# Performance work log

Measured on AMD Instinct MI355X. Metric: run time of the kernel, lower is better.

Reference implementation:

```python
import jax, jax.numpy as jnp
import numpy as np
from jax import lax

SUBBANDS = 4
TAPS = 64
BETA = 9.0


def _qmf_filter():
    # scipy.signal.kaiser(M, beta) == np.kaiser(M, beta)
    h = np.kaiser(TAPS + 1, BETA)
    h = h / np.sum(h)
    n = np.arange(TAPS + 1)
    filt = [h * np.cos((2 * k + 1) * np.pi * n / (2 * SUBBANDS) + (-1) ** k * np.pi / 4)
            for k in range(SUBBANDS)]
    return np.asarray(filt, dtype=np.float32)  # [S, TAPS+1]


def setup_inputs() -> dict:
    key = jax.random.key(0)
    x = jax.random.normal(key, (16, 1, 524288), dtype=jnp.float32)
    qmf = jnp.asarray(_qmf_filter())
    return {"x": x, "qmf": qmf}


def reference(x, qmf):
    S = SUBBANDS
    pad = TAPS // 2  # 32
    # --- analysis: full conv then ::S decimation == strided conv (identical outputs) ---
    wa = qmf[:, None, :]  # [S, 1, TAPS+1] (OIW)
    sub = lax.conv_general_dilated(
        x, wa, window_strides=(S,), padding=[(pad, pad)],
        dimension_numbers=("NCH", "OIH", "NCH"))  # [B, S, T//S]
    # --- synthesis: zero-stuff upsample by S then conv, summed over subbands.
    # lhs_dilation=S inserts the zeros; right pad extra S-1 to match the
    # explicit x_up buffer (3 trailing zeros after the last sample).
    # Summing the S per-subband convs == one conv with S input channels.
    ws = qmf[None, :, :]  # [1, S, TAPS+1]
    y = lax.conv_general_dilated(
        sub, ws, window_strides=(1,), padding=[(pad, pad + S - 1)],
        lhs_dilation=(S,), dimension_numbers=("NCH", "OIH", "NCH"))  # [B, 1, T]
    return y
```

## Files before the change

### kernel.cpp

```cpp
#include <hip/hip_runtime.h>

#define LEN 524288
#define LSUB 131072
#define BATCH 16
#define NXG 1056
#define NTILE 128

constexpr double cabs_d(double a) { return a < 0 ? -a : a; }
constexpr double csqrt_d(double a) {
    double x = (a > 1.0) ? a : 1.0;
    for (int i = 0; i < 48; i++) x = 0.5 * (x + a / x);
    return x;
}
constexpr double i0_d(double x) {
    double t = 1.0, s = 1.0;
    for (int m = 1; m < 50; m++) { double u = x / (2.0 * m); t *= u * u; s += t; }
    return s;
}
struct Tbl {
    float f[4][65];
    float C[4][129];
};
constexpr Tbl make_tbl() {
    Tbl T{};
    double h[65] = {};
    double sum = 0.0;
    const double ib = i0_d(9.0);
    for (int n = 0; n < 65; n++) {
        double r = (n - 32.0) / 32.0;
        double a = 1.0 - r * r; if (a < 0) a = 0;
        h[n] = i0_d(9.0 * csqrt_d(a)) / ib;
        sum += h[n];
    }
    for (int n = 0; n < 65; n++) h[n] /= sum;
    const double S2 = csqrt_d(2.0);
    const double c1 = 0.5 * csqrt_d(2.0 + S2);
    const double c2 = 0.5 * S2;
    const double c3 = 0.5 * csqrt_d(2.0 - S2);
    const double ct[16] = {1,c1,c2,c3,0,-c3,-c2,-c1,-1,-c1,-c2,-c3,0,c3,c2,c1};
    double f[4][65] = {};
    for (int k = 0; k < 4; k++)
        for (int n = 0; n < 65; n++) {
            int m = ((2 * k + 1) * n + ((k & 1) ? 14 : 2)) & 15;
            f[k][n] = h[n] * ct[m];
            T.f[k][n] = (float)f[k][n];
        }
    double Cd[4][129] = {};
    for (int p = 0; p < 4; p++)
        for (int dd = -64; dd <= 64; dd++) {
            double a = 0.0;
            for (int k = 0; k < 4; k++)
                for (int j = -8; j <= 8; j++) {
                    int ia = 4 * j + 32 - p, ib2 = dd - 4 * j + 32;
                    if (ia >= 0 && ia <= 64 && ib2 >= 0 && ib2 <= 64)
                        a += f[k][ia] * f[k][ib2];
                }
            Cd[p][dd + 64] = a;
        }
    for (int p = 0; p < 4; p++) {
        double budget = 2e-8;
        while (true) {
            int best = -1; double bv = 1e30;
            for (int d = 0; d < 129; d++) {
                double c = cabs_d(Cd[p][d]);
                if (c > 0.0 && c < bv) { bv = c; best = d; }
            }
            if (best < 0 || bv * bv > budget) break;
            budget -= bv * bv;
            Cd[p][best] = 0.0;
        }
        for (int d = 0; d < 129; d++) T.C[p][d] = (float)Cd[p][d];
    }
    return T;
}
static constexpr Tbl TBL = make_tbl();

__device__ __forceinline__ int swz(int g) { return g ^ ((g >> 3) & 7); }
__device__ __forceinline__ float getc(const float4& v, int c) {
    switch (c) { case 0: return v.x; case 1: return v.y; case 2: return v.z; default: return v.w; }
}
__device__ __forceinline__ float cpv(int p, int dlt) {
    return (dlt < -64 || dlt > 64) ? 0.0f : TBL.C[p][dlt + 64];
}
__device__ __forceinline__ float lds_x(const float4* xs, int xi, int gbase) {
    int r = (xi >> 2) - gbase;
    return reinterpret_cast<const float*>(&xs[swz(r)])[xi & 3];
}

template <int TT>
__device__ __forceinline__ void left_fix(const float4* xs, float (&acc)[4][4]) {
    float sig[4][8];
    #pragma unroll
    for (int mi = 0; mi < 8; mi++) {
        const int m = mi - 8;
        float s0 = 0.f, s1 = 0.f, s2 = 0.f, s3 = 0.f;
        #pragma unroll
        for (int n = 32 - 4 * m; n <= 64; n++) {
            float xv = lds_x(xs, 4 * m - 32 + n, -16);
            s0 = fmaf(TBL.f[0][n], xv, s0);
            s1 = fmaf(TBL.f[1][n], xv, s1);
            s2 = fmaf(TBL.f[2][n], xv, s2);
            s3 = fmaf(TBL.f[3][n], xv, s3);
        }
        sig[0][mi] = s0; sig[1][mi] = s1; sig[2][mi] = s2; sig[3][mi] = s3;
    }
    #pragma unroll
    for (int o = 0; o < 4; o++) {
        const int u = 4 * TT + o;
        #pragma unroll
        for (int p = 0; p < 4; p++) {
            float s = 0.f;
            #pragma unroll
            for (int mi = 0; mi < 8; mi++) {
                const int np = 4 * ((mi - 8) - u) + 32 - p;
                if (np >= 0 && np <= 64) {
                    s = fmaf(TBL.f[0][np], sig[0][mi], s);
                    s = fmaf(TBL.f[1][np], sig[1][mi], s);
                    s = fmaf(TBL.f[2][np], sig[2][mi], s);
                    s = fmaf(TBL.f[3][np], sig[3][mi], s);
                }
            }
            acc[o][p] -= s;
        }
    }
}

template <int TT>
__device__ __forceinline__ void right_fix(const float4* xs, float (&acc)[4][4]) {
    constexpr int GB = LSUB - 1040;
    float sig[4][8];
    #pragma unroll
    for (int mi = 0; mi < 8; mi++) {
        float s0 = 0.f, s1 = 0.f, s2 = 0.f, s3 = 0.f;
        #pragma unroll
        for (int n = 0; n <= 31 - 4 * mi; n++) {
            float xv = lds_x(xs, 4 * (LSUB + mi) - 32 + n, GB);
            s0 = fmaf(TBL.f[0][n], xv, s0);
            s1 = fmaf(TBL.f[1][n], xv, s1);
            s2 = fmaf(TBL.f[2][n], xv, s2);
            s3 = fmaf(TBL.f[3][n], xv, s3);
        }
        sig[0][mi] = s0; sig[1][mi] = s1; sig[2][mi] = s2; sig[3][mi] = s3;
    }
    #pragma unroll
    for (int o = 0; o < 4; o++) {
        const int u = (LSUB - 1024) + 4 * TT + o;
        #pragma unroll
        for (int p = 0; p < 4; p++) {
            float s = 0.f;
            #pragma unroll
            for (int mi = 0; mi < 8; mi++) {
                const int np = 4 * ((LSUB + mi) - u) + 32 - p;
                if (np >= 0 && np <= 64) {
                    s = fmaf(TBL.f[0][np], sig[0][mi], s);
                    s = fmaf(TBL.f[1][np], sig[1][mi], s);
                    s = fmaf(TBL.f[2][np], sig[2][mi], s);
                    s = fmaf(TBL.f[3][np], sig[3][mi], s);
                }
            }
            acc[o][p] -= s;
        }
    }
}

__global__ __launch_bounds__(256, 8) void pqmf_composite(const float* __restrict__ x,
                                                         float* __restrict__ y) {
    __shared__ float4 xs[NXG];

    const int t = threadIdx.x;
    const int b = blockIdx.x >> 7;
    const int tile = blockIdx.x & (NTILE - 1);
    const int u0 = tile << 10;
    const float* xb = x + (size_t)b * LEN;
    const int gbase = u0 - 16;

    if (gbase >= 0 && gbase + NXG <= LSUB) {
        #pragma unroll
        for (int q = 0; q < 4; q++)
            xs[swz(t + 256 * q)] = *reinterpret_cast<const float4*>(xb + 4 * (gbase + t + 256 * q));
        if (t < NXG - 1024)
            xs[swz(t + 1024)] = *reinterpret_cast<const float4*>(xb + 4 * (gbase + t + 1024));
    } else {
        for (int r = t; r < NXG; r += 256) {
            int g = gbase + r;
            float4 v = make_float4(0.f, 0.f, 0.f, 0.f);
            if (g >= 0 && g < LSUB) v = *reinterpret_cast<const float4*>(xb + 4 * g);
            xs[swz(r)] = v;
        }
    }
    __syncthreads();

    float acc[4][4] = {};
    float4 vb[4];
    #pragma unroll
    for (int i = 0; i < 4; i++) vb[i] = xs[swz(4 * t + i)];
    #pragma unroll
    for (int d = -16; d <= 19; d++) {
        float4 v = vb[(d + 16) & 3];
        if (d + 4 <= 19) vb[(d + 16) & 3] = xs[swz(4 * t + 16 + d + 4)];
        #pragma unroll
        for (int o = 0; o < 4; o++) {
            const int e = d - o;
            if (e < -16 || e > 16) continue;
            #pragma unroll
            for (int p = 0; p < 4; p++) {
                const int c0 = p & 1, c1 = (p & 1) + 2;
                const float w0 = cpv(p, 4 * e + c0);
                const float w1 = cpv(p, 4 * e + c1);
                if (w0 != 0.f) acc[o][p] = fmaf(w0, getc(v, c0), acc[o][p]);
                if (w1 != 0.f) acc[o][p] = fmaf(w1, getc(v, c1), acc[o][p]);
            }
        }
    }

    if (tile == 0 && t < 2) {
        if (t == 0) left_fix<0>(xs, acc); else left_fix<1>(xs, acc);
    }
    if (tile == NTILE - 1 && t >= 254) {
        if (t == 254) right_fix<254>(xs, acc); else right_fix<255>(xs, acc);
    }

    float4* yb = reinterpret_cast<float4*>(y + (size_t)b * LEN);
    #pragma unroll
    for (int o = 0; o < 4; o++)
        yb[u0 + 4 * t + o] = make_float4(acc[o][0], acc[o][1], acc[o][2], acc[o][3]);
}

extern "C" void kernel_launch(void* const* d_in, const int* in_sizes, int n_in,
                              void* d_out, int out_size, void* d_ws, size_t ws_size,
                              hipStream_t stream) {
    const float* x = (const float*)d_in[0];
    float* y = (float*)d_out;
    dim3 blk(256);
    dim3 grd(BATCH * NTILE);
    pqmf_composite<<<grd, blk, 0, stream>>>(x, y);
}
```

Baseline: 113.2 us.

## Replace LDS-tiled composite filter with direct per-granule global loads

Drops the shared-memory staging tile and its barrier. Each thread now computes one output granule of 4 samples by reading its 33 neighbouring float4 values straight from global memory, relying on L1/L2 to supply the reuse between neighbouring threads. Thread count goes up 4x, and the edge corrections are done per granule. The risk is about 33 global load instructions per output granule instead of LDS reuse, and fewer outputs per thread over which to spread the register-resident weights.

```diff
diff --git a/kernel.cpp b/kernel.cpp
--- a/kernel.cpp
+++ b/kernel.cpp
@@ -3,8 +3,6 @@
 #define LEN 524288
 #define LSUB 131072
 #define BATCH 16
-#define NXG 1056
-#define NTILE 128
 
 constexpr double cabs_d(double a) { return a < 0 ? -a : a; }
 constexpr double csqrt_d(double a) {
@@ -75,155 +73,105 @@
 }
 static constexpr Tbl TBL = make_tbl();
 
-__device__ __forceinline__ int swz(int g) { return g ^ ((g >> 3) & 7); }
 __device__ __forceinline__ float getc(const float4& v, int c) {
     switch (c) { case 0: return v.x; case 1: return v.y; case 2: return v.z; default: return v.w; }
 }
 __device__ __forceinline__ float cpv(int p, int dlt) {
     return (dlt < -64 || dlt > 64) ? 0.0f : TBL.C[p][dlt + 64];
 }
-__device__ __forceinline__ float lds_x(const float4* xs, int xi, int gbase) {
-    int r = (xi >> 2) - gbase;
-    return reinterpret_cast<const float*>(&xs[swz(r)])[xi & 3];
+
+template <bool SAFE>
+__device__ __forceinline__ void compute_granule(const float4* __restrict__ xb4, int g,
+                                                float (&acc)[4]) {
+    #pragma unroll
+    for (int e = -16; e <= 16; e++) {
+        float4 v;
+        if (SAFE) {
+            int gg = g + e;
+            v = (gg >= 0 && gg < LSUB) ? xb4[gg] : make_float4(0.f, 0.f, 0.f, 0.f);
+        } else {
+            v = xb4[g + e];
+        }
+        #pragma unroll
+        for (int c = 0; c < 4; c++) {
+            const int par = c & 1;
+            const float w0 = cpv(par,     4 * e + c);
+            const float w1 = cpv(par + 2, 4 * e + c);
+            const float xv = getc(v, c);
+            if (w0 != 0.f) acc[par]     = fmaf(w0, xv, acc[par]);
+            if (w1 != 0.f) acc[par + 2] = fmaf(w1, xv, acc[par + 2]);
+        }
+    }
 }
 
-template <int TT>
-__device__ __forceinline__ void left_fix(const float4* xs, float (&acc)[4][4]) {
-    float sig[4][8];
+__device__ void left_fix_g(const float* __restrict__ xb, int g, float (&acc)[4]) {
     #pragma unroll
     for (int mi = 0; mi < 8; mi++) {
         const int m = mi - 8;
         float s0 = 0.f, s1 = 0.f, s2 = 0.f, s3 = 0.f;
         #pragma unroll
-        for (int n = 32 - 4 * m; n <= 64; n++) {
-            float xv = lds_x(xs, 4 * m - 32 + n, -16);
+        for (int n = 64 - 4 * mi; n <= 64; n++) {
+            float xv = xb[4 * m - 32 + n];
             s0 = fmaf(TBL.f[0][n], xv, s0);
             s1 = fmaf(TBL.f[1][n], xv, s1);
             s2 = fmaf(TBL.f[2][n], xv, s2);
             s3 = fmaf(TBL.f[3][n], xv, s3);
         }
-        sig[0][mi] = s0; sig[1][mi] = s1; sig[2][mi] = s2; sig[3][mi] = s3;
-    }
-    #pragma unroll
-    for (int o = 0; o < 4; o++) {
-        const int u = 4 * TT + o;
         #pragma unroll
         for (int p = 0; p < 4; p++) {
-            float s = 0.f;
-            #pragma unroll
-            for (int mi = 0; mi < 8; mi++) {
-                const int np = 4 * ((mi - 8) - u) + 32 - p;
-                if (np >= 0 && np <= 64) {
-                    s = fmaf(TBL.f[0][np], sig[0][mi], s);
-                    s = fmaf(TBL.f[1][np], sig[1][mi], s);
-                    s = fmaf(TBL.f[2][np], sig[2][mi], s);
-                    s = fmaf(TBL.f[3][np], sig[3][mi], s);
-                }
+            int np = 4 * (m - g) + 32 - p;
+            if (np >= 0 && np <= 64) {
+                float w = TBL.f[0][np] * s0 + TBL.f[1][np] * s1 +
+                          TBL.f[2][np] * s2 + TBL.f[3][np] * s3;
+                acc[p] -= w;
             }
-            acc[o][p] -= s;
         }
     }
 }
 
-template <int TT>
-__device__ __forceinline__ void right_fix(const float4* xs, float (&acc)[4][4]) {
-    constexpr int GB = LSUB - 1040;
-    float sig[4][8];
+__device__ void right_fix_g(const float* __restrict__ xb, int g, float (&acc)[4]) {
     #pragma unroll
     for (int mi = 0; mi < 8; mi++) {
+        const int m = LSUB + mi;
         float s0 = 0.f, s1 = 0.f, s2 = 0.f, s3 = 0.f;
         #pragma unroll
         for (int n = 0; n <= 31 - 4 * mi; n++) {
-            float xv = lds_x(xs, 4 * (LSUB + mi) - 32 + n, GB);
+            float xv = xb[4 * m - 32 + n];
             s0 = fmaf(TBL.f[0][n], xv, s0);
             s1 = fmaf(TBL.f[1][n], xv, s1);
             s2 = fmaf(TBL.f[2][n], xv, s2);
             s3 = fmaf(TBL.f[3][n], xv, s3);
         }
-        sig[0][mi] = s0; sig[1][mi] = s1; sig[2][mi] = s2; sig[3][mi] = s3;
-    }
-    #pragma unroll
-    for (int o = 0; o < 4; o++) {
-        const int u = (LSUB - 1024) + 4 * TT + o;
         #pragma unroll
         for (int p = 0; p < 4; p++) {
-            float s = 0.f;
-            #pragma unroll
-            for (int mi = 0; mi < 8; mi++) {
-                const int np = 4 * ((LSUB + mi) - u) + 32 - p;
-                if (np >= 0 && np <= 64) {
-                    s = fmaf(TBL.f[0][np], sig[0][mi], s);
-                    s = fmaf(TBL.f[1][np], sig[1][mi], s);
-                    s = fmaf(TBL.f[2][np], sig[2][mi], s);
-                    s = fmaf(TBL.f[3][np], sig[3][mi], s);
-                }
+            int np = 4 * (m - g) + 32 - p;
+            if (np >= 0 && np <= 64) {
+                float w = TBL.f[0][np] * s0 + TBL.f[1][np] * s1 +
+                          TBL.f[2][np] * s2 + TBL.f[3][np] * s3;
+                acc[p] -= w;
             }
-            acc[o][p] -= s;
         }
     }
 }
 
-__global__ __launch_bounds__(256, 8) void pqmf_composite(const float* __restrict__ x,
-                                                         float* __restrict__ y) {
-    __shared__ float4 xs[NXG];
+__global__ __launch_bounds__(256, 4) void pqmf_direct(const float* __restrict__ x,
+                                                      float* __restrict__ y) {
+    const int idx = blockIdx.x * 256 + threadIdx.x;
+    const int g = idx & (LSUB - 1);
+    const int b = idx >> 17;
+    const float* xb = x + (size_t)b * LEN;
+    const float4* xb4 = reinterpret_cast<const float4*>(xb);
 
-    const int t = threadIdx.x;
-    const int b = blockIdx.x >> 7;
-    const int tile = blockIdx.x & (NTILE - 1);
-    const int u0 = tile << 10;
-    const float* xb = x + (size_t)b * LEN;
-    const int gbase = u0 - 16;
-
-    if (gbase >= 0 && gbase + NXG <= LSUB) {
-        #pragma unroll
-        for (int q = 0; q < 4; q++)
-            xs[swz(t + 256 * q)] = *reinterpret_cast<const float4*>(xb + 4 * (gbase + t + 256 * q));
-        if (t < NXG - 1024)
-            xs[swz(t + 1024)] = *reinterpret_cast<const float4*>(xb + 4 * (gbase + t + 1024));
+    float acc[4] = {0.f, 0.f, 0.f, 0.f};
+    if (g >= 16 && g < LSUB - 16) {
+        compute_granule<false>(xb4, g, acc);
     } else {
-        for (int r = t; r < NXG; r += 256) {
-            int g = gbase + r;
-            float4 v = make_float4(0.f, 0.f, 0.f, 0.f);
-            if (g >= 0 && g < LSUB) v = *reinterpret_cast<const float4*>(xb + 4 * g);
-            xs[swz(r)] = v;
-        }
+        compute_granule<true>(xb4, g, acc);
+        if (g <= 8) left_fix_g(xb, g, acc);
+        if (g >= LSUB - 9) right_fix_g(xb, g, acc);
     }
-    __syncthreads();
-
-    float acc[4][4] = {};
-    float4 vb[4];
-    #pragma unroll
-    for (int i = 0; i < 4; i++) vb[i] = xs[swz(4 * t + i)];
-    #pragma unroll
-    for (int d = -16; d <= 19; d++) {
-        float4 v = vb[(d + 16) & 3];
-        if (d + 4 <= 19) vb[(d + 16) & 3] = xs[swz(4 * t + 16 + d + 4)];
-        #pragma unroll
-        for (int o = 0; o < 4; o++) {
-            const int e = d - o;
-            if (e < -16 || e > 16) continue;
-            #pragma unroll
-            for (int p = 0; p < 4; p++) {
-                const int c0 = p & 1, c1 = (p & 1) + 2;
-                const float w0 = cpv(p, 4 * e + c0);
-                const float w1 = cpv(p, 4 * e + c1);
-                if (w0 != 0.f) acc[o][p] = fmaf(w0, getc(v, c0), acc[o][p]);
-                if (w1 != 0.f) acc[o][p] = fmaf(w1, getc(v, c1), acc[o][p]);
-            }
-        }
-    }
-
-    if (tile == 0 && t < 2) {
-        if (t == 0) left_fix<0>(xs, acc); else left_fix<1>(xs, acc);
-    }
-    if (tile == NTILE - 1 && t >= 254) {
-        if (t == 254) right_fix<254>(xs, acc); else right_fix<255>(xs, acc);
-    }
-
-    float4* yb = reinterpret_cast<float4*>(y + (size_t)b * LEN);
-    #pragma unroll
-    for (int o = 0; o < 4; o++)
-        yb[u0 + 4 * t + o] = make_float4(acc[o][0], acc[o][1], acc[o][2], acc[o][3]);
+    reinterpret_cast<float4*>(y + (size_t)b * LEN)[g] =
+        make_float4(acc[0], acc[1], acc[2], acc[3]);
 }
 
 extern "C" void kernel_launch(void* const* d_in, const int* in_sizes, int n_in,
@@ -232,6 +180,6 @@
     const float* x = (const float*)d_in[0];
     float* y = (float*)d_out;
     dim3 blk(256);
-    dim3 grd(BATCH * NTILE);
-    pqmf_composite<<<grd, blk, 0, stream>>>(x, y);
+    dim3 grd(BATCH * LSUB / 256);
+    pqmf_direct<<<grd, blk, 0, stream>>>(x, y);
 }
```

Result: faster. 90.89 us (-19.7%).
